# Optimization experiments

Hardware: AMD Instinct MI355X
Metric: run time of the kernel (lower is better)

Reference implementation:

```python
import jax, jax.numpy as jnp
import numpy as np

EMB = 768
HEADS = 8

def setup_inputs() -> dict:
    key = jax.random.key(0)
    ks = jax.random.split(key, 9)
    B, N, E = 16, 1024, EMB
    s = 1.0 / np.sqrt(E)
    x = jax.random.normal(ks[0], (B, N, E), dtype=jnp.float32)
    Wq = jax.random.normal(ks[1], (E, E), dtype=jnp.float32) * s
    bq = jnp.zeros((E,), dtype=jnp.float32)
    Wk = jax.random.normal(ks[2], (E, E), dtype=jnp.float32) * s
    bk = jnp.zeros((E,), dtype=jnp.float32)
    Wv = jax.random.normal(ks[3], (E, E), dtype=jnp.float32) * s
    bv = jnp.zeros((E,), dtype=jnp.float32)
    Wo = jax.random.normal(ks[4], (E, E), dtype=jnp.float32) * s
    bo = jnp.zeros((E,), dtype=jnp.float32)
    return {"x": x, "Wq": Wq, "bq": bq, "Wk": Wk, "bk": bk, "Wv": Wv, "bv": bv, "Wo": Wo, "bo": bo}

def reference(x, Wq, bq, Wk, bk, Wv, bv, Wo, bo):
    B, N, E = x.shape
    H = HEADS
    D = E // H
    # separate Q/K/V linears, split heads: b n (h d) -> b h n d
    q = (x @ Wq + bq).reshape(B, N, H, D).transpose(0, 2, 1, 3)
    k = (x @ Wk + bk).reshape(B, N, H, D).transpose(0, 2, 1, 3)
    v = (x @ Wv + bv).reshape(B, N, H, D).transpose(0, 2, 1, 3)
    energy = jnp.einsum('bhqd,bhkd->bhqk', q, k)
    # NON-STANDARD: softmax first, then divide by sqrt(emb_size)
    scaling = jnp.float32(E) ** 0.5
    attn = jax.nn.softmax(energy, axis=-1) / scaling
    out = jnp.einsum('bhqk,bhkd->bhqd', attn, v)
    out = out.transpose(0, 2, 1, 3).reshape(B, N, E)  # b h n d -> b n (h d)
    return out @ Wo + bo
```

## Files before the change

### kernel.cpp

```cpp
#include <hip/hip_runtime.h>


typedef _Float16 half8 __attribute__((ext_vector_type(8)));
typedef __fp16 fp16x2 __attribute__((ext_vector_type(2)));
typedef float f32x4 __attribute__((ext_vector_type(4)));
typedef float f32x16 __attribute__((ext_vector_type(16)));

__device__ __forceinline__ void gload_lds16(const void* g, void* l) {
  __builtin_amdgcn_global_load_lds((const __attribute__((address_space(1))) void*)g,
                                   (__attribute__((address_space(3))) void*)l, 16, 0, 0);
}


__global__ __launch_bounds__(256) void conv_x_kernel(const float* __restrict__ x,
                                                     _Float16* __restrict__ xh) {
  long i = ((long)blockIdx.x * 256 + threadIdx.x) * 8;
  float4 a = *(const float4*)(x + i);
  float4 b = *(const float4*)(x + i + 4);
  half8 o;
  o[0] = (_Float16)a.x; o[1] = (_Float16)a.y; o[2] = (_Float16)a.z; o[3] = (_Float16)a.w;
  o[4] = (_Float16)b.x; o[5] = (_Float16)b.y; o[6] = (_Float16)b.z; o[7] = (_Float16)b.w;
  *(half8*)(xh + i) = o;
}

__global__ __launch_bounds__(256) void transpose_cvt_kernel(
    const float* __restrict__ W0, const float* __restrict__ W1,
    const float* __restrict__ W2, const float* __restrict__ W3,
    _Float16* __restrict__ WT) {
  __shared__ float tile[32][33];
  int z = blockIdx.z;
  const float* W = (z == 0) ? W0 : (z == 1) ? W1 : (z == 2) ? W2 : W3;
  int k0 = blockIdx.y * 32, n0 = blockIdx.x * 32;
  int tx = threadIdx.x, ty = threadIdx.y;
#pragma unroll
  for (int j = ty; j < 32; j += 8)
    tile[j][tx] = W[(size_t)(k0 + j) * 768 + n0 + tx];
  __syncthreads();
  _Float16* dst = WT + (size_t)z * 768 * 768;
#pragma unroll
  for (int j = ty; j < 32; j += 8)
    dst[(size_t)(n0 + j) * 768 + k0 + tx] = (_Float16)tile[tx][j];
}


template <int OUT_F16>
__global__ __launch_bounds__(256) void gemm_nt_kernel(
    const _Float16* __restrict__ A, const _Float16* __restrict__ Bt,
    const float* __restrict__ b0, const float* __restrict__ b1,
    const float* __restrict__ b2, void* __restrict__ C,
    int M, int N, int K, int ldc) {
  __shared__ _Float16 As[128 * 64];
  __shared__ _Float16 Bs[128 * 64];
  int nbx = N >> 7;
  int nwg = gridDim.x;
  int wg = blockIdx.x;
  int cpx = nwg >> 3;
  int swz = (wg & 7) * cpx + (wg >> 3);
  int bx = swz % nbx, by = swz / nbx;
  int m0 = by * 128, n0 = bx * 128;
  int t = threadIdx.x, l = t & 63, w = t >> 6;
  int lg = l >> 4, lr = l & 15;
  int wr = w >> 1, wc = w & 1;
  f32x4 acc[4][4] = {};

  int srow[4], ssc[4];
#pragma unroll
  for (int j = 0; j < 4; ++j) {
    int s = j * 256 + t;
    srow[j] = s >> 3;
    ssc[j] = ((s & 7) ^ (srow[j] & 7)) * 8;
  }

  for (int k0 = 0; k0 < K; k0 += 64) {
    __syncthreads();
#pragma unroll
    for (int j = 0; j < 4; ++j)
      gload_lds16(A + (size_t)(m0 + srow[j]) * K + k0 + ssc[j], &As[(j * 256 + t) * 8]);
#pragma unroll
    for (int j = 0; j < 4; ++j)
      gload_lds16(Bt + (size_t)(n0 + srow[j]) * K + k0 + ssc[j], &Bs[(j * 256 + t) * 8]);
    __syncthreads();

#pragma unroll
    for (int kk = 0; kk < 2; ++kk) {
      half8 af[4], bf[4];
#pragma unroll
      for (int r = 0; r < 4; ++r) {
        int row = wr * 64 + r * 16 + lr;
        af[r] = *(const half8*)&As[row * 64 + (((kk * 4 + lg) ^ (row & 7)) * 8)];
      }
#pragma unroll
      for (int c = 0; c < 4; ++c) {
        int row = wc * 64 + c * 16 + lr;
        bf[c] = *(const half8*)&Bs[row * 64 + (((kk * 4 + lg) ^ (row & 7)) * 8)];
      }
#pragma unroll
      for (int r = 0; r < 4; ++r)
#pragma unroll
        for (int c = 0; c < 4; ++c)
          acc[r][c] = __builtin_amdgcn_mfma_f32_16x16x32_f16(af[r], bf[c], acc[r][c], 0, 0, 0);
    }
  }

#pragma unroll
  for (int r = 0; r < 4; ++r)
#pragma unroll
    for (int c = 0; c < 4; ++c) {
      int col = n0 + wc * 64 + c * 16 + lr;
      float bb = (col < 768) ? b0[col] : (col < 1536) ? b1[col - 768] : b2[col - 1536];
#pragma unroll
      for (int i = 0; i < 4; ++i) {
        int row = m0 + wr * 64 + r * 16 + lg * 4 + i;
        float v = acc[r][c][i] + bb;
        if (OUT_F16)
          ((_Float16*)C)[(size_t)row * ldc + col] = (_Float16)v;
        else
          ((float*)C)[(size_t)row * ldc + col] = v;
      }
    }
}


__global__ __launch_bounds__(256, 2) void attn_kernel(const _Float16* __restrict__ QKV,
                                                      _Float16* __restrict__ Oh) {
  int hw = blockIdx.x;
  int lin = (hw & 7) * 128 + (hw >> 3);
  int bh = lin >> 3, qt = lin & 7;
  int b = bh >> 3, h = bh & 7;
  int t = threadIdx.x, w = t >> 6, l = t & 63;
  int lr = l & 31, hi = l >> 5;

  __shared__ __align__(16) char KF[2][12288];
  __shared__ __align__(16) _Float16 VF[2][96 * 64];

  const _Float16* Qb = QKV + (size_t)b * 1024 * 2304 + h * 96;
  const _Float16* Kb = Qb + 768;
  const _Float16* Vb = Qb + 1536;

  half8 qf[6];
  {
    int qrow = qt * 128 + w * 32 + lr;
    const _Float16 s = (_Float16)1.4426950408889634f;
#pragma unroll
    for (int c = 0; c < 6; ++c) {
      qf[c] = *(const half8*)&Qb[(size_t)qrow * 2304 + c * 16 + hi * 8];
#pragma unroll
      for (int e = 0; e < 8; ++e) qf[c][e] = qf[c][e] * s;
    }
  }

  int ks_src[3], ks_dst[3];
#pragma unroll
  for (int j = 0; j < 3; ++j) {
    int s = j * 256 + t;
    int f = s >> 6, lane = s & 63;
    int sb = f / 6, c = f - sb * 6;
    ks_src[j] = (sb * 32 + (lane & 31)) * 2304 + c * 16 + ((lane >> 5) & 1) * 8;
    ks_dst[j] = s * 16;
  }
  bool vact[2];
  int v_src[2], v_dst[2][8];
#pragma unroll
  for (int j = 0; j < 2; ++j) {
    int u = j * 256 + t;
    vact[j] = u < 384;
    int kvp = u / 12, mm = u % 12;
    v_src[j] = 2 * kvp * 2304 + mm * 8;
#pragma unroll
    for (int e = 0; e < 8; ++e) {
      int d = mm * 8 + e;
      int sw = ((d & 7) ^ ((d >> 3) & 7)) << 3;
      v_dst[j][e] = d * 64 + ((2 * kvp) ^ sw);
    }
  }

  auto stage_K = [&](int kv0, int bi) {
    size_t goff = (size_t)kv0 * 2304;
#pragma unroll
    for (int j = 0; j < 3; ++j)
      gload_lds16(Kb + goff + ks_src[j], &KF[bi][ks_dst[j]]);
  };

  half8 vr0[2], vr1[2];
  auto loadV = [&](int kv0) {
    size_t goff = (size_t)kv0 * 2304;
#pragma unroll
    for (int j = 0; j < 2; ++j)
      if (vact[j]) {
        const _Float16* vp = Vb + goff + v_src[j];
        vr0[j] = *(const half8*)vp;
        vr1[j] = *(const half8*)(vp + 2304);
      }
  };
  auto writeV = [&](int bi) {
#pragma unroll
    for (int j = 0; j < 2; ++j)
      if (vact[j]) {
#pragma unroll
        for (int e = 0; e < 8; ++e) {
          union { _Float16 h2[2]; unsigned u32; } pk;
          pk.h2[0] = vr0[j][e]; pk.h2[1] = vr1[j][e];
          *(unsigned*)&VF[bi][v_dst[j][e]] = pk.u32;
        }
      }
  };

  half8 vones;
#pragma unroll
  for (int e = 0; e < 8; ++e) vones[e] = (_Float16)1.0f;

  float m_run = -3.0e38f;
  f32x16 oa[3] = {};
  f32x16 lacc = {};

  stage_K(0, 0);
  loadV(0);
  writeV(0);

  for (int tile = 0; tile < 16; ++tile) {
    int bi = tile & 1;
    __syncthreads();
    if (tile + 1 < 16) {
      stage_K((tile + 1) * 64, bi ^ 1);
      loadV((tile + 1) * 64);
      __builtin_amdgcn_sched_barrier(0);
    }

    f32x16 sA[2] = {};
#pragma unroll
    for (int sb = 0; sb < 2; ++sb)
#pragma unroll
      for (int c = 0; c < 6; ++c) {
        half8 kf = *(const half8*)(KF[bi] + (sb * 6 + c) * 1024 + l * 16);
        sA[sb] = __builtin_amdgcn_mfma_f32_32x32x16_f16(kf, qf[c], sA[sb], 0, 0, 0);
      }

    float tmax = -3.0e38f;
#pragma unroll
    for (int sb = 0; sb < 2; ++sb)
#pragma unroll
      for (int r = 0; r < 16; ++r) tmax = fmaxf(tmax, sA[sb][r]);
    tmax = fmaxf(tmax, __shfl_xor(tmax, 32, 64));

    if (!__all(tmax <= m_run + 11.5f)) {
      float m_new = fmaxf(m_run, tmax);
      float scale = __builtin_exp2f(m_run - m_new);
#pragma unroll
      for (int r = 0; r < 16; ++r) {
        float sr = __shfl(scale, (r & 3) + 8 * (r >> 2) + 4 * hi, 64);
        oa[0][r] *= sr; oa[1][r] *= sr; oa[2][r] *= sr;
        lacc[r] *= sr;
      }
      m_run = m_new;
    }

    unsigned keep[8], send[8];
#pragma unroll
    for (int sb = 0; sb < 2; ++sb) {
      float e[16];
#pragma unroll
      for (int r = 0; r < 16; ++r) e[r] = __builtin_exp2f(sA[sb][r] - m_run);
      unsigned w32[8];
#pragma unroll
      for (int p = 0; p < 4; ++p)
#pragma unroll
        for (int m = 0; m < 2; ++m) {
          union { fp16x2 h2; unsigned u; } pk;
          pk.h2 = __builtin_amdgcn_cvt_pkrtz(e[4 * p + 2 * m], e[4 * p + 2 * m + 1]);
          w32[p * 2 + m] = pk.u;
        }
#pragma unroll
      for (int kb = 0; kb < 2; ++kb)
#pragma unroll
        for (int m = 0; m < 2; ++m) {
          keep[sb * 4 + kb * 2 + m] = hi ? w32[(2 * kb + 1) * 2 + m] : w32[(2 * kb) * 2 + m];
          send[sb * 4 + kb * 2 + m] = hi ? w32[(2 * kb) * 2 + m] : w32[(2 * kb + 1) * 2 + m];
        }
    }

    unsigned recv[8];
#pragma unroll
    for (int i = 0; i < 8; ++i) recv[i] = __shfl_xor(send[i], 32, 64);

#pragma unroll
    for (int kstep = 0; kstep < 4; ++kstep) {
      int base = (kstep >> 1) * 4 + (kstep & 1) * 2;
      union { unsigned u[4]; half8 h8; } pa;
      pa.u[0] = hi ? recv[base + 0] : keep[base + 0];
      pa.u[1] = hi ? recv[base + 1] : keep[base + 1];
      pa.u[2] = hi ? keep[base + 0] : recv[base + 0];
      pa.u[3] = hi ? keep[base + 1] : recv[base + 1];
#pragma unroll
      for (int dt = 0; dt < 3; ++dt) {
        int d = dt * 32 + lr;
        int sw = ((d & 7) ^ ((d >> 3) & 7)) << 3;
        half8 vf = *(const half8*)&VF[bi][d * 64 + ((kstep * 16 + hi * 8) ^ sw)];
        oa[dt] = __builtin_amdgcn_mfma_f32_32x32x16_f16(pa.h8, vf, oa[dt], 0, 0, 0);
      }
      lacc = __builtin_amdgcn_mfma_f32_32x32x16_f16(pa.h8, vones, lacc, 0, 0, 0);
    }

    if (tile + 1 < 16) writeV(bi ^ 1);
  }

  size_t rbase = (size_t)(b * 1024 + qt * 128 + w * 32) * 768 + h * 96;
#pragma unroll
  for (int r = 0; r < 16; ++r) {
    int q = (r & 3) + 8 * (r >> 2) + 4 * hi;
    float ivr = 1.0f / (lacc[r] * 27.712812921102035f);
#pragma unroll
    for (int dt = 0; dt < 3; ++dt)
      Oh[rbase + (size_t)q * 768 + dt * 32 + lr] = (_Float16)(oa[dt][r] * ivr);
  }
}


extern "C" void kernel_launch(void* const* d_in, const int* in_sizes, int n_in,
                              void* d_out, int out_size, void* d_ws, size_t ws_size,
                              hipStream_t stream) {
  const float* x  = (const float*)d_in[0];
  const float* Wq = (const float*)d_in[1];
  const float* bq = (const float*)d_in[2];
  const float* Wk = (const float*)d_in[3];
  const float* bk = (const float*)d_in[4];
  const float* Wv = (const float*)d_in[5];
  const float* bv = (const float*)d_in[6];
  const float* Wo = (const float*)d_in[7];
  const float* bo = (const float*)d_in[8];
  float* out = (float*)d_out;

  char* ws = (char*)d_ws;
  _Float16* WT   = (_Float16*)(ws);
  _Float16* xh   = (_Float16*)(ws + 4751360);
  _Float16* QKV  = (_Float16*)(ws + 29917184);
  _Float16* Oh   = (_Float16*)(ws + 105414656);

  conv_x_kernel<<<6144, 256, 0, stream>>>(x, xh);
  transpose_cvt_kernel<<<dim3(24, 24, 4), dim3(32, 8), 0, stream>>>(Wq, Wk, Wv, Wo, WT);

  gemm_nt_kernel<1><<<2304, 256, 0, stream>>>(xh, WT, bq, bk, bv, QKV,
                                              16384, 2304, 768, 2304);

  attn_kernel<<<1024, 256, 0, stream>>>(QKV, Oh);

  gemm_nt_kernel<0><<<768, 256, 0, stream>>>(Oh, WT + (size_t)2304 * 768, bo, bo, bo, out,
                                             16384, 768, 768, 768);
}
```

Baseline: 227.5 us.

## Rewrite projection GEMM as 256x256 double-buffered 8-wave kernel with interleaved prefetch

Replaces the 128x128 single-buffered GEMM with a 256x256 tile, 512-thread kernel. It double-buffers LDS and issues the next k-tile's global-to-LDS loads in the middle of the MFMA phases, with barriers and raised scheduling priority around the math. The goal is to hide global load latency and get more reuse per byte loaded. In exchange it uses 128KB of LDS per block and leaves fewer blocks in the grid (576 and 192), so the out-projection may underfill the 256 CUs.

```diff
diff --git a/kernel.cpp b/kernel.cpp
--- a/kernel.cpp
+++ b/kernel.cpp
@@ -44,74 +44,109 @@
 
 
 template <int OUT_F16>
-__global__ __launch_bounds__(256) void gemm_nt_kernel(
+__global__ __launch_bounds__(512) void gemm8p_kernel(
     const _Float16* __restrict__ A, const _Float16* __restrict__ Bt,
     const float* __restrict__ b0, const float* __restrict__ b1,
     const float* __restrict__ b2, void* __restrict__ C,
     int M, int N, int K, int ldc) {
-  __shared__ _Float16 As[128 * 64];
-  __shared__ _Float16 Bs[128 * 64];
-  int nbx = N >> 7;
-  int nwg = gridDim.x;
-  int wg = blockIdx.x;
+  __shared__ _Float16 As[2][256 * 64];
+  __shared__ _Float16 Bs[2][256 * 64];
+  int nbx = N >> 8;
+  int nwg = gridDim.x, wg = blockIdx.x;
   int cpx = nwg >> 3;
   int swz = (wg & 7) * cpx + (wg >> 3);
   int bx = swz % nbx, by = swz / nbx;
-  int m0 = by * 128, n0 = bx * 128;
+  int m0 = by * 256, n0 = bx * 256;
   int t = threadIdx.x, l = t & 63, w = t >> 6;
   int lg = l >> 4, lr = l & 15;
-  int wr = w >> 1, wc = w & 1;
-  f32x4 acc[4][4] = {};
+  int wm = w >> 2, wn = w & 3;
+  f32x4 acc[8][4] = {};
 
   int srow[4], ssc[4];
 #pragma unroll
   for (int j = 0; j < 4; ++j) {
-    int s = j * 256 + t;
+    int s = j * 512 + t;
     srow[j] = s >> 3;
     ssc[j] = ((s & 7) ^ (srow[j] & 7)) * 8;
   }
 
-  for (int k0 = 0; k0 < K; k0 += 64) {
-    __syncthreads();
+  auto stageA = [&](int kt, int c) {
+    int k0 = kt * 64;
 #pragma unroll
     for (int j = 0; j < 4; ++j)
-      gload_lds16(A + (size_t)(m0 + srow[j]) * K + k0 + ssc[j], &As[(j * 256 + t) * 8]);
+      gload_lds16(A + (size_t)(m0 + srow[j]) * K + k0 + ssc[j], &As[c][(j * 512 + t) * 8]);
+  };
+  auto stageB = [&](int kt, int c) {
+    int k0 = kt * 64;
 #pragma unroll
     for (int j = 0; j < 4; ++j)
-      gload_lds16(Bt + (size_t)(n0 + srow[j]) * K + k0 + ssc[j], &Bs[(j * 256 + t) * 8]);
-    __syncthreads();
-
-#pragma unroll
-    for (int kk = 0; kk < 2; ++kk) {
-      half8 af[4], bf[4];
-#pragma unroll
-      for (int r = 0; r < 4; ++r) {
-        int row = wr * 64 + r * 16 + lr;
-        af[r] = *(const half8*)&As[row * 64 + (((kk * 4 + lg) ^ (row & 7)) * 8)];
-      }
-#pragma unroll
-      for (int c = 0; c < 4; ++c) {
-        int row = wc * 64 + c * 16 + lr;
-        bf[c] = *(const half8*)&Bs[row * 64 + (((kk * 4 + lg) ^ (row & 7)) * 8)];
-      }
-#pragma unroll
-      for (int r = 0; r < 4; ++r)
-#pragma unroll
-        for (int c = 0; c < 4; ++c)
-          acc[r][c] = __builtin_amdgcn_mfma_f32_16x16x32_f16(af[r], bf[c], acc[r][c], 0, 0, 0);
-    }
-  }
-
-#pragma unroll
-  for (int r = 0; r < 4; ++r)
-#pragma unroll
-    for (int c = 0; c < 4; ++c) {
-      int col = n0 + wc * 64 + c * 16 + lr;
+      gload_lds16(Bt + (size_t)(n0 + srow[j]) * K + k0 + ssc[j], &Bs[c][(j * 512 + t) * 8]);
+  };
+
+  stageA(0, 0); stageB(0, 0);
+  asm volatile("s_waitcnt vmcnt(0)" ::: "memory");
+  __builtin_amdgcn_sched_barrier(0);
+  __builtin_amdgcn_s_barrier();
+
+  int nkt = K >> 6;
+  for (int kt = 0; kt < nkt; ++kt) {
+    int c = kt & 1;
+    bool pre = (kt + 1) < nkt;
+    half8 bf[4][2];
+#pragma unroll
+    for (int qd = 0; qd < 4; ++qd) {
+      half8 af[2][2];
+      if (qd == 0) {
+#pragma unroll
+        for (int fc = 0; fc < 4; ++fc)
+#pragma unroll
+          for (int kk = 0; kk < 2; ++kk) {
+            int row = wn * 64 + fc * 16 + lr;
+            bf[fc][kk] = *(const half8*)&Bs[c][row * 64 + (((kk * 4 + lg) ^ (row & 7)) * 8)];
+          }
+      }
+#pragma unroll
+      for (int f2 = 0; f2 < 2; ++f2)
+#pragma unroll
+        for (int kk = 0; kk < 2; ++kk) {
+          int row = wm * 128 + (qd * 2 + f2) * 16 + lr;
+          af[f2][kk] = *(const half8*)&As[c][row * 64 + (((kk * 4 + lg) ^ (row & 7)) * 8)];
+        }
+      if (qd == 0 && pre) stageA(kt + 1, c ^ 1);
+      if (qd == 1 && pre) stageB(kt + 1, c ^ 1);
+      __builtin_amdgcn_sched_barrier(0);
+      __builtin_amdgcn_s_barrier();
+      asm volatile("s_waitcnt lgkmcnt(0)" ::: "memory");
+      __builtin_amdgcn_sched_barrier(0);
+      __builtin_amdgcn_s_setprio(1);
+#pragma unroll
+      for (int f2 = 0; f2 < 2; ++f2)
+#pragma unroll
+        for (int fc = 0; fc < 4; ++fc)
+#pragma unroll
+          for (int kk = 0; kk < 2; ++kk)
+            acc[qd * 2 + f2][fc] = __builtin_amdgcn_mfma_f32_16x16x32_f16(
+                af[f2][kk], bf[fc][kk], acc[qd * 2 + f2][fc], 0, 0, 0);
+      __builtin_amdgcn_s_setprio(0);
+      __builtin_amdgcn_sched_barrier(0);
+      if (qd == 3) {
+        asm volatile("s_waitcnt vmcnt(0)" ::: "memory");
+        __builtin_amdgcn_sched_barrier(0);
+      }
+      __builtin_amdgcn_s_barrier();
+    }
+  }
+
+#pragma unroll
+  for (int fr = 0; fr < 8; ++fr)
+#pragma unroll
+    for (int fc = 0; fc < 4; ++fc) {
+      int col = n0 + wn * 64 + fc * 16 + lr;
       float bb = (col < 768) ? b0[col] : (col < 1536) ? b1[col - 768] : b2[col - 1536];
 #pragma unroll
       for (int i = 0; i < 4; ++i) {
-        int row = m0 + wr * 64 + r * 16 + lg * 4 + i;
-        float v = acc[r][c][i] + bb;
+        int row = m0 + wm * 128 + fr * 16 + lg * 4 + i;
+        float v = acc[fr][fc][i] + bb;
         if (OUT_F16)
           ((_Float16*)C)[(size_t)row * ldc + col] = (_Float16)v;
         else
@@ -338,11 +373,11 @@
   conv_x_kernel<<<6144, 256, 0, stream>>>(x, xh);
   transpose_cvt_kernel<<<dim3(24, 24, 4), dim3(32, 8), 0, stream>>>(Wq, Wk, Wv, Wo, WT);
 
-  gemm_nt_kernel<1><<<2304, 256, 0, stream>>>(xh, WT, bq, bk, bv, QKV,
-                                              16384, 2304, 768, 2304);
+  gemm8p_kernel<1><<<576, 512, 0, stream>>>(xh, WT, bq, bk, bv, QKV,
+                                            16384, 2304, 768, 2304);
 
   attn_kernel<<<1024, 256, 0, stream>>>(QKV, Oh);
 
-  gemm_nt_kernel<0><<<768, 256, 0, stream>>>(Oh, WT + (size_t)2304 * 768, bo, bo, bo, out,
-                                             16384, 768, 768, 768);
-}
+  gemm8p_kernel<0><<<192, 512, 0, stream>>>(Oh, WT + (size_t)2304 * 768, bo, bo, bo, out,
+                                            16384, 768, 768, 768);
+}
```

After: 236.0 us. +3.8%, slower.

## Double attention block size to 256 query rows across 8 waves

Applied to the files above, without the earlier changes.

The attention kernel now launches 512 blocks of 512 threads, each covering 256 query rows with eight waves instead of 128 rows with four. Each K/V tile staged in shared memory is reused by twice as many waves, which halves global K/V traffic per query and spreads the staging work over more threads (two K loads and one V load per thread). In exchange each block holds more resources, there are fewer blocks to fill the GPU, and register pressure rises under the 512-thread launch bound.

```diff
diff --git a/kernel.cpp b/kernel.cpp
--- a/kernel.cpp
+++ b/kernel.cpp
@@ -121,11 +121,11 @@
 }
 
 
-__global__ __launch_bounds__(256, 2) void attn_kernel(const _Float16* __restrict__ QKV,
+__global__ __launch_bounds__(512, 2) void attn_kernel(const _Float16* __restrict__ QKV,
                                                       _Float16* __restrict__ Oh) {
   int hw = blockIdx.x;
-  int lin = (hw & 7) * 128 + (hw >> 3);
-  int bh = lin >> 3, qt = lin & 7;
+  int lin = (hw & 7) * 64 + (hw >> 3);
+  int bh = lin >> 2, qt = lin & 3;
   int b = bh >> 3, h = bh & 7;
   int t = threadIdx.x, w = t >> 6, l = t & 63;
   int lr = l & 31, hi = l >> 5;
@@ -139,7 +139,7 @@
 
   half8 qf[6];
   {
-    int qrow = qt * 128 + w * 32 + lr;
+    int qrow = qt * 256 + w * 32 + lr;
     const _Float16 s = (_Float16)1.4426950408889634f;
 #pragma unroll
     for (int c = 0; c < 6; ++c) {
@@ -149,60 +149,55 @@
     }
   }
 
-  int ks_src[3], ks_dst[3];
-#pragma unroll
-  for (int j = 0; j < 3; ++j) {
-    int s = j * 256 + t;
+  auto kslot = [](int s, int& src, int& dst) {
     int f = s >> 6, lane = s & 63;
     int sb = f / 6, c = f - sb * 6;
-    ks_src[j] = (sb * 32 + (lane & 31)) * 2304 + c * 16 + ((lane >> 5) & 1) * 8;
-    ks_dst[j] = s * 16;
-  }
-  bool vact[2];
-  int v_src[2], v_dst[2][8];
-#pragma unroll
-  for (int j = 0; j < 2; ++j) {
-    int u = j * 256 + t;
-    vact[j] = u < 384;
-    int kvp = u / 12, mm = u % 12;
-    v_src[j] = 2 * kvp * 2304 + mm * 8;
+    src = (sb * 32 + (lane & 31)) * 2304 + c * 16 + ((lane >> 5) & 1) * 8;
+    dst = s * 16;
+  };
+  int k1_src, k1_dst;
+  kslot(t, k1_src, k1_dst);
+  bool k2on = t < 256;
+  int k2_src = 0, k2_dst = 0;
+  if (k2on) kslot(512 + t, k2_src, k2_dst);
+
+  bool von = (t >= 256) || (t < 128);
+  int vu = (t >= 256) ? (t - 256) : (256 + t);
+  int v_src = 0, v_dst[8] = {};
+  {
+    int kvp = vu / 12, mm = vu % 12;
+    v_src = 2 * kvp * 2304 + mm * 8;
 #pragma unroll
     for (int e = 0; e < 8; ++e) {
       int d = mm * 8 + e;
       int sw = ((d & 7) ^ ((d >> 3) & 7)) << 3;
-      v_dst[j][e] = d * 64 + ((2 * kvp) ^ sw);
+      v_dst[e] = d * 64 + ((2 * kvp) ^ sw);
     }
   }
 
   auto stage_K = [&](int kv0, int bi) {
     size_t goff = (size_t)kv0 * 2304;
-#pragma unroll
-    for (int j = 0; j < 3; ++j)
-      gload_lds16(Kb + goff + ks_src[j], &KF[bi][ks_dst[j]]);
+    gload_lds16(Kb + goff + k1_src, &KF[bi][k1_dst]);
+    if (k2on) gload_lds16(Kb + goff + k2_src, &KF[bi][k2_dst]);
   };
 
-  half8 vr0[2], vr1[2];
+  half8 vr0, vr1;
   auto loadV = [&](int kv0) {
-    size_t goff = (size_t)kv0 * 2304;
-#pragma unroll
-    for (int j = 0; j < 2; ++j)
-      if (vact[j]) {
-        const _Float16* vp = Vb + goff + v_src[j];
-        vr0[j] = *(const half8*)vp;
-        vr1[j] = *(const half8*)(vp + 2304);
-      }
+    if (von) {
+      const _Float16* vp = Vb + (size_t)kv0 * 2304 + v_src;
+      vr0 = *(const half8*)vp;
+      vr1 = *(const half8*)(vp + 2304);
+    }
   };
   auto writeV = [&](int bi) {
-#pragma unroll
-    for (int j = 0; j < 2; ++j)
-      if (vact[j]) {
-#pragma unroll
-        for (int e = 0; e < 8; ++e) {
-          union { _Float16 h2[2]; unsigned u32; } pk;
-          pk.h2[0] = vr0[j][e]; pk.h2[1] = vr1[j][e];
-          *(unsigned*)&VF[bi][v_dst[j][e]] = pk.u32;
-        }
-      }
+    if (von) {
+#pragma unroll
+      for (int e = 0; e < 8; ++e) {
+        union { _Float16 h2[2]; unsigned u32; } pk;
+        pk.h2[0] = vr0[e]; pk.h2[1] = vr1[e];
+        *(unsigned*)&VF[bi][v_dst[e]] = pk.u32;
+      }
+    }
   };
 
   half8 vones;
@@ -303,7 +298,7 @@
     if (tile + 1 < 16) writeV(bi ^ 1);
   }
 
-  size_t rbase = (size_t)(b * 1024 + qt * 128 + w * 32) * 768 + h * 96;
+  size_t rbase = (size_t)(b * 1024 + qt * 256 + w * 32) * 768 + h * 96;
 #pragma unroll
   for (int r = 0; r < 16; ++r) {
     int q = (r & 3) + 8 * (r >> 2) + 4 * hi;
@@ -341,7 +336,7 @@
   gemm_nt_kernel<1><<<2304, 256, 0, stream>>>(xh, WT, bq, bk, bv, QKV,
                                               16384, 2304, 768, 2304);
 
-  attn_kernel<<<1024, 256, 0, stream>>>(QKV, Oh);
+  attn_kernel<<<512, 512, 0, stream>>>(QKV, Oh);
 
   gemm_nt_kernel<0><<<768, 256, 0, stream>>>(Oh, WT + (size_t)2304 * 768, bo, bo, bo, out,
                                              16384, 768, 768, 768);
```

New measurement: 231.1 us. Within noise of the previous version (+1.6%).
